# Optimization experiments

Measured on AMD Instinct MI355X. Metric: run time of the kernel, lower is better.

## Reference

```python
import jax, jax.numpy as jnp
import numpy as np

L = 7          # window side (odd)
A = 0.3        # weight of average term
B = 0.7        # weight of differential term


def mex_hat(d):
    grid = (np.mgrid[:d, :d] - d // 2) * 1.0
    eucl = np.sqrt((grid ** 2).sum(0)) / d
    return (eucl * np.exp(-eucl)).astype(np.float32)  # (d, d)


def setup_inputs() -> dict:
    key = jax.random.key(0)
    x = jax.random.normal(key, (64, 1, 512, 512), dtype=jnp.float32)
    kernel = jnp.asarray(mex_hat(L).reshape(-1))  # (L*L,), matches unfold row-major order
    return {"x": x, "kernel": kernel}


def reference(x, kernel):
    # x: [B,1,n,n], kernel: [L*L]
    n = x.shape[2]
    pad = L // 2
    xp = jnp.pad(x, ((0, 0), (0, 0), (pad, pad), (pad, pad)))  # zero pad, as F.unfold
    mean_acc = jnp.zeros_like(x)
    diff_acc = jnp.zeros_like(x)
    # fixed 49-offset loop replaces the im2col buffer; each shift is a view-slice
    for i in range(L):
        for j in range(L):
            s = jax.lax.dynamic_slice(xp, (0, 0, i, j), x.shape)
            mean_acc = mean_acc + s
            diff_acc = diff_acc + kernel[i * L + j] * jax.nn.relu(s - x)
    average_term = jnp.exp(-mean_acc / (L * L))              # [B,1,n,n]
    differential_term = diff_acc                             # [B,1,n,n]
    mask = A * average_term + B * differential_term
    mask = mask / jnp.sqrt(jnp.sum(mask ** 2))               # global L2 norm
    out = jnp.where(x > mask, x, jnp.zeros_like(x))
    return out, average_term, differential_term
```

## Files before the change

### kernel.cpp

```cpp
#include <hip/hip_runtime.h>
#include <stdint.h>

#define IMG 512
constexpr int TX = 64, TY = 32, PADW = 3;
constexpr int SMW = TX + 2 * PADW;
constexpr int SMH = TY + 2 * PADW;
constexpr int SMS = SMW + 2;
constexpr float A_W = 0.3f, B_W = 0.7f;

#define W1  0.12383970f
#define W2  0.16507309f
#define W4  0.21470754f
#define W5  0.23209061f
#define W8  0.26975268f
#define W9  0.27918814f
#define W10 0.28754623f
#define W13 0.30773566f
#define W18 0.33061044f

__device__ constexpr float KW[7][7] = {
    { W18, W13, W10, W9,  W10, W13, W18 },
    { W13, W8,  W5,  W4,  W5,  W8,  W13 },
    { W10, W5,  W2,  W1,  W2,  W5,  W10 },
    { W9,  W4,  W1,  0.f, W1,  W4,  W9  },
    { W10, W5,  W2,  W1,  W2,  W5,  W10 },
    { W13, W8,  W5,  W4,  W5,  W8,  W13 },
    { W18, W13, W10, W9,  W10, W13, W18 },
};

constexpr float ksum_calc() {
    float s = 0.f;
    for (int i = 0; i < 7; ++i)
        for (int j = 0; j < 7; ++j) s += KW[i][j];
    return s;
}
constexpr float KSUM = ksum_calc();

__global__ __launch_bounds__(256) void li_pass1(
    const float* __restrict__ x,
    float* __restrict__ outMask,
    float* __restrict__ outAvg,
    float* __restrict__ outDiff,
    float* __restrict__ partials)
{
    __shared__ float sm[SMH * SMS];
    __shared__ float red[4];
    const int tid = threadIdx.x;

    const int bx = blockIdx.x, by = blockIdx.y, b = blockIdx.z;
    const size_t imgBase = (size_t)b * IMG * IMG;
    const int x0 = bx * TX, y0 = by * TY;

    for (int idx = tid; idx < SMH * SMW; idx += 256) {
        int ly = idx / SMW, lx = idx - ly * SMW;
        int gx = x0 - PADW + lx, gy = y0 - PADW + ly;
        float v = 0.f;
        if ((unsigned)gx < IMG && (unsigned)gy < IMG)
            v = x[imgBase + (size_t)gy * IMG + gx];
        sm[ly * SMS + lx] = v;
    }
    __syncthreads();

    const int tx  = tid & 63;
    const int r   = tid >> 6;
    const int ty0 = r * 8;

    float c[8], mean[8], T[8];
    #pragma unroll
    for (int k = 0; k < 8; ++k) {
        c[k] = sm[(ty0 + k + PADW) * SMS + tx + PADW];
        mean[k] = 0.f; T[k] = 0.f;
    }

    #pragma unroll
    for (int wy = 0; wy < 14; ++wy) {
        float s[7];
        const int base = (ty0 + wy) * SMS + tx;
        #pragma unroll
        for (int dx = 0; dx < 7; ++dx) s[dx] = sm[base + dx];
        float rowsum = ((s[0] + s[1]) + (s[2] + s[3])) + ((s[4] + s[5]) + s[6]);
        #pragma unroll
        for (int k = 0; k < 8; ++k) {
            const int dy = wy - k;
            if (dy >= 0 && dy < 7) {
                mean[k] += rowsum;
                #pragma unroll
                for (int dx = 0; dx < 7; ++dx) {
                    if (KW[dy][dx] != 0.f)
                        T[k] = fmaf(KW[dy][dx], fmaxf(s[dx], c[k]), T[k]);
                }
            }
        }
    }

    float local = 0.f;
    #pragma unroll
    for (int k = 0; k < 8; ++k) {
        float avg = __expf(mean[k] * (-1.f / 49.f));
        float d   = fmaf(-KSUM, c[k], T[k]);
        float m   = fmaf(A_W, avg, B_W * d);
        local = fmaf(m, m, local);
        size_t g = imgBase + (size_t)(y0 + ty0 + k) * IMG + (x0 + tx);
        outAvg[g]  = avg;
        outDiff[g] = d;
        outMask[g] = m;
    }

    float v = local;
    #pragma unroll
    for (int off = 32; off > 0; off >>= 1) v += __shfl_down(v, off);
    if ((tid & 63) == 0) red[tid >> 6] = v;
    __syncthreads();
    if (tid == 0) {
        size_t pb = ((size_t)b * gridDim.y + by) * gridDim.x + bx;
        partials[pb] = red[0] + red[1] + red[2] + red[3];
    }
}

__global__ __launch_bounds__(1024) void li_reduce(
    const float* __restrict__ partials, int n, float* __restrict__ total)
{
    __shared__ float red[16];
    int tid = threadIdx.x;
    float v = 0.f;
    for (int i = tid; i < n; i += 1024) v += partials[i];
    #pragma unroll
    for (int off = 32; off > 0; off >>= 1) v += __shfl_down(v, off);
    if ((tid & 63) == 0) red[tid >> 6] = v;
    __syncthreads();
    if (tid == 0) {
        float s = 0.f;
        #pragma unroll
        for (int i = 0; i < 16; ++i) s += red[i];
        *total = s;
    }
}

__global__ __launch_bounds__(256) void li_pass2(
    const float4* __restrict__ x, const float4* __restrict__ mask,
    float4* __restrict__ out, const float* __restrict__ total)
{
    const float inv = 1.0f / sqrtf(*total);
    int i = blockIdx.x * 256 + threadIdx.x;
    float4 xv = x[i];
    float4 mv = mask[i];
    float4 ov;
    ov.x = (xv.x > mv.x * inv) ? xv.x : 0.f;
    ov.y = (xv.y > mv.y * inv) ? xv.y : 0.f;
    ov.z = (xv.z > mv.z * inv) ? xv.z : 0.f;
    ov.w = (xv.w > mv.w * inv) ? xv.w : 0.f;
    out[i] = ov;
}

extern "C" void kernel_launch(void* const* d_in, const int* in_sizes, int n_in,
                              void* d_out, int out_size, void* d_ws, size_t ws_size,
                              hipStream_t stream)
{
    const float* x = (const float*)d_in[0];
    const int Nelem = in_sizes[0];
    const int batch = Nelem / (IMG * IMG);

    float* out     = (float*)d_out;
    float* outMask = out;
    float* outAvg  = out + (size_t)Nelem;
    float* outDiff = out + (size_t)2 * Nelem;

    float* partials = (float*)d_ws;
    const int nblocks = (IMG / TX) * (IMG / TY) * batch;
    float* total = partials + nblocks;

    dim3 g1(IMG / TX, IMG / TY, batch);
    li_pass1<<<g1, 256, 0, stream>>>(x, outMask, outAvg, outDiff, partials);
    li_reduce<<<1, 1024, 0, stream>>>(partials, nblocks, total);

    const int nvec = Nelem / 4;
    li_pass2<<<nvec / 256, 256, 0, stream>>>(
        (const float4*)x, (const float4*)outMask, (float4*)out, total);
}
```

Measured before the change: 308.0 us.

## Fuse stencil, norm reduction and threshold into one cooperative grid-sync kernel

Replaces the three-kernel pipeline with one cooperative kernel. Each block processes eight vertical tiles, keeps its mask values in registers packed as bf16 pairs, and does a grid-wide sync after writing partial sums. Every block then re-reduces the partials and applies the threshold directly, so the full-precision mask is never written to global memory and read back, and two launches go away. The costs are fewer, longer-running blocks with a high register load, and threshold comparisons made against a bf16-rounded mask, which can flip elements that lie near the threshold. The old three-kernel path stays as a fallback if the cooperative launch fails.

```diff
diff --git a/kernel.cpp b/kernel.cpp
--- a/kernel.cpp
+++ b/kernel.cpp
@@ -1,12 +1,15 @@
 #include <hip/hip_runtime.h>
+#include <hip/hip_cooperative_groups.h>
 #include <stdint.h>
 
 #define IMG 512
-constexpr int TX = 64, TY = 32, PADW = 3;
+constexpr int PADW = 3;
+constexpr float A_W = 0.3f, B_W = 0.7f;
+
+constexpr int TX = 64, TY = 32;
 constexpr int SMW = TX + 2 * PADW;
 constexpr int SMH = TY + 2 * PADW;
 constexpr int SMS = SMW + 2;
-constexpr float A_W = 0.3f, B_W = 0.7f;
 
 #define W1  0.12383970f
 #define W2  0.16507309f
@@ -36,17 +39,151 @@
 }
 constexpr float KSUM = ksum_calc();
 
-__global__ __launch_bounds__(256) void li_pass1(
+__device__ __forceinline__ float asf(unsigned u) {
+    union { unsigned u; float f; } c; c.u = u; return c.f;
+}
+__device__ __forceinline__ unsigned f2bf_bits(float f) {
+    union { float f; unsigned u; } c; c.f = f;
+    unsigned u = c.u;
+    return (u + 0x7fffu + ((u >> 16) & 1u)) >> 16;
+}
+
+__global__ __launch_bounds__(256, 4) void li_fused(
     const float* __restrict__ x,
-    float* __restrict__ outMask,
+    float* __restrict__ outThr,
     float* __restrict__ outAvg,
     float* __restrict__ outDiff,
     float* __restrict__ partials)
 {
     __shared__ float sm[SMH * SMS];
     __shared__ float red[4];
+    __shared__ float s_inv;
+
     const int tid = threadIdx.x;
-
+    const int bx = blockIdx.x, by = blockIdx.y, b = blockIdx.z;
+    const size_t imgBase = (size_t)b * IMG * IMG;
+    const int x0 = bx * TX;
+    const int yBase = by * 256;
+
+    const int tx  = tid & 63;
+    const int r   = tid >> 6;
+    const int ty0 = r * 8;
+
+    unsigned mp[32];
+    float local = 0.f;
+
+    #pragma unroll
+    for (int s = 0; s < 8; ++s) {
+        const int y0 = yBase + s * TY;
+
+        if (s > 0) __syncthreads();
+        for (int idx = tid; idx < SMH * SMW; idx += 256) {
+            int ly = idx / SMW, lx = idx - ly * SMW;
+            int gx = x0 - PADW + lx, gy = y0 - PADW + ly;
+            float v = 0.f;
+            if ((unsigned)gx < IMG && (unsigned)gy < IMG)
+                v = x[imgBase + (size_t)gy * IMG + gx];
+            sm[ly * SMS + lx] = v;
+        }
+        __syncthreads();
+
+        float c[8], mean[8], T[8];
+        #pragma unroll
+        for (int k = 0; k < 8; ++k) {
+            c[k] = sm[(ty0 + k + PADW) * SMS + tx + PADW];
+            mean[k] = 0.f; T[k] = 0.f;
+        }
+
+        #pragma unroll
+        for (int wy = 0; wy < 14; ++wy) {
+            float sv[7];
+            const int base = (ty0 + wy) * SMS + tx;
+            #pragma unroll
+            for (int dx = 0; dx < 7; ++dx) sv[dx] = sm[base + dx];
+            float rowsum = ((sv[0] + sv[1]) + (sv[2] + sv[3])) + ((sv[4] + sv[5]) + sv[6]);
+            #pragma unroll
+            for (int k = 0; k < 8; ++k) {
+                const int dy = wy - k;
+                if (dy >= 0 && dy < 7) {
+                    mean[k] += rowsum;
+                    #pragma unroll
+                    for (int dx = 0; dx < 7; ++dx) {
+                        if (KW[dy][dx] != 0.f)
+                            T[k] = fmaf(KW[dy][dx], fmaxf(sv[dx], c[k]), T[k]);
+                    }
+                }
+            }
+        }
+
+        float m8[8];
+        #pragma unroll
+        for (int k = 0; k < 8; ++k) {
+            float avg = __expf(mean[k] * (-1.f / 49.f));
+            float d   = fmaf(-KSUM, c[k], T[k]);
+            float m   = fmaf(A_W, avg, B_W * d);
+            m8[k] = m;
+            local = fmaf(m, m, local);
+            size_t g = imgBase + (size_t)(y0 + ty0 + k) * IMG + (x0 + tx);
+            outAvg[g]  = avg;
+            outDiff[g] = d;
+        }
+        #pragma unroll
+        for (int k = 0; k < 8; k += 2)
+            mp[s * 4 + k / 2] = f2bf_bits(m8[k]) | (f2bf_bits(m8[k + 1]) << 16);
+    }
+
+    {
+        float v = local;
+        #pragma unroll
+        for (int off = 32; off > 0; off >>= 1) v += __shfl_down(v, off);
+        if ((tid & 63) == 0) red[tid >> 6] = v;
+        __syncthreads();
+        if (tid == 0) {
+            int pb = (b * (int)gridDim.y + by) * (int)gridDim.x + bx;
+            partials[pb] = red[0] + red[1] + red[2] + red[3];
+        }
+    }
+
+    __threadfence();
+    cooperative_groups::this_grid().sync();
+
+    {
+        const int nPart = (int)(gridDim.x * gridDim.y * gridDim.z);
+        float v = 0.f;
+        for (int i = tid; i < nPart; i += 256) v += partials[i];
+        #pragma unroll
+        for (int off = 32; off > 0; off >>= 1) v += __shfl_down(v, off);
+        if ((tid & 63) == 0) red[tid >> 6] = v;
+        __syncthreads();
+        if (tid == 0) s_inv = 1.0f / sqrtf(red[0] + red[1] + red[2] + red[3]);
+        __syncthreads();
+    }
+    const float inv = s_inv;
+
+    #pragma unroll
+    for (int s = 0; s < 8; ++s) {
+        #pragma unroll
+        for (int k = 0; k < 8; k += 2) {
+            unsigned pk = mp[s * 4 + k / 2];
+            float m0 = asf(pk << 16);
+            float m1 = asf(pk & 0xffff0000u);
+            size_t g = imgBase + (size_t)(yBase + s * TY + ty0 + k) * IMG + (x0 + tx);
+            float xv0 = x[g];
+            float xv1 = x[g + IMG];
+            outThr[g]       = (xv0 > m0 * inv) ? xv0 : 0.f;
+            outThr[g + IMG] = (xv1 > m1 * inv) ? xv1 : 0.f;
+        }
+    }
+}
+
+__global__ __launch_bounds__(256) void li_pass1(
+    const float* __restrict__ x,
+    float* __restrict__ outMask, float* __restrict__ outAvg,
+    float* __restrict__ outDiff, float* __restrict__ partials)
+{
+    __shared__ float sm[SMH * SMS];
+    __shared__ float red[4];
+    const int tid = threadIdx.x;
     const int bx = blockIdx.x, by = blockIdx.y, b = blockIdx.z;
     const size_t imgBase = (size_t)b * IMG * IMG;
     const int x0 = bx * TX, y0 = by * TY;
@@ -61,8 +198,8 @@
     }
     __syncthreads();
 
-    const int tx  = tid & 63;
-    const int r   = tid >> 6;
+    const int tx = tid & 63;
+    const int r  = tid >> 6;
     const int ty0 = r * 8;
 
     float c[8], mean[8], T[8];
@@ -71,28 +208,25 @@
         c[k] = sm[(ty0 + k + PADW) * SMS + tx + PADW];
         mean[k] = 0.f; T[k] = 0.f;
     }
-
     #pragma unroll
     for (int wy = 0; wy < 14; ++wy) {
-        float s[7];
+        float sv[7];
         const int base = (ty0 + wy) * SMS + tx;
         #pragma unroll
-        for (int dx = 0; dx < 7; ++dx) s[dx] = sm[base + dx];
-        float rowsum = ((s[0] + s[1]) + (s[2] + s[3])) + ((s[4] + s[5]) + s[6]);
+        for (int dx = 0; dx < 7; ++dx) sv[dx] = sm[base + dx];
+        float rowsum = ((sv[0] + sv[1]) + (sv[2] + sv[3])) + ((sv[4] + sv[5]) + sv[6]);
         #pragma unroll
         for (int k = 0; k < 8; ++k) {
             const int dy = wy - k;
             if (dy >= 0 && dy < 7) {
                 mean[k] += rowsum;
                 #pragma unroll
-                for (int dx = 0; dx < 7; ++dx) {
+                for (int dx = 0; dx < 7; ++dx)
                     if (KW[dy][dx] != 0.f)
-                        T[k] = fmaf(KW[dy][dx], fmaxf(s[dx], c[k]), T[k]);
-                }
+                        T[k] = fmaf(KW[dy][dx], fmaxf(sv[dx], c[k]), T[k]);
             }
         }
     }
-
     float local = 0.f;
     #pragma unroll
     for (int k = 0; k < 8; ++k) {
@@ -101,11 +235,8 @@
         float m   = fmaf(A_W, avg, B_W * d);
         local = fmaf(m, m, local);
         size_t g = imgBase + (size_t)(y0 + ty0 + k) * IMG + (x0 + tx);
-        outAvg[g]  = avg;
-        outDiff[g] = d;
-        outMask[g] = m;
-    }
-
+        outAvg[g] = avg; outDiff[g] = d; outMask[g] = m;
+    }
     float v = local;
     #pragma unroll
     for (int off = 32; off > 0; off >>= 1) v += __shfl_down(v, off);
@@ -161,19 +292,27 @@
     const int batch = Nelem / (IMG * IMG);
 
     float* out     = (float*)d_out;
-    float* outMask = out;
     float* outAvg  = out + (size_t)Nelem;
     float* outDiff = out + (size_t)2 * Nelem;
-
     float* partials = (float*)d_ws;
-    const int nblocks = (IMG / TX) * (IMG / TY) * batch;
-    float* total = partials + nblocks;
-
-    dim3 g1(IMG / TX, IMG / TY, batch);
-    li_pass1<<<g1, 256, 0, stream>>>(x, outMask, outAvg, outDiff, partials);
-    li_reduce<<<1, 1024, 0, stream>>>(partials, nblocks, total);
-
-    const int nvec = Nelem / 4;
-    li_pass2<<<nvec / 256, 256, 0, stream>>>(
-        (const float4*)x, (const float4*)outMask, (float4*)out, total);
-}
+
+    dim3 gridF(IMG / TX, IMG / 256, batch);
+    dim3 blockF(256, 1, 1);
+    void* args[] = { (void*)&x, (void*)&out, (void*)&outAvg,
+                     (void*)&outDiff, (void*)&partials };
+    hipError_t err = hipLaunchCooperativeKernel(
+        (const void*)li_fused, gridF, blockF, args, 0, stream);
+
+    if (err != hipSuccess) {
+        (void)hipGetLastError();
+        float* outMask = out;
+        const int nblocks = (IMG / TX) * (IMG / TY) * batch;
+        float* total = partials + nblocks;
+        dim3 g1(IMG / TX, IMG / TY, batch);
+        li_pass1<<<g1, 256, 0, stream>>>(x, outMask, outAvg, outDiff, partials);
+        li_reduce<<<1, 1024, 0, stream>>>(partials, nblocks, total);
+        const int nvec = Nelem / 4;
+        li_pass2<<<nvec / 256, 256, 0, stream>>>(
+            (const float4*)x, (const float4*)outMask, (float4*)out, total);
+    }
+}
```

Measured after the change: 610.9 us. 1.98x slower.

## Register-block 4x4 outputs per thread with float4 LDS and global access

Applied to the files above, without the earlier changes.

Each thread now computes a 4x4 output patch from a 128x32 tile instead of an 8x1 column. Shared-memory rows are loaded and read with float4 vectors, row sums are computed with a sliding window, and outputs are written as float4. This is meant to cut LDS traffic per output and global instruction count. In exchange it raises register pressure (48 accumulators) under a launch-bounds occupancy hint and adds a separate halo load path.

```diff
diff --git a/kernel.cpp b/kernel.cpp
--- a/kernel.cpp
+++ b/kernel.cpp
@@ -2,10 +2,9 @@
 #include <stdint.h>
 
 #define IMG 512
-constexpr int TX = 64, TY = 32, PADW = 3;
-constexpr int SMW = TX + 2 * PADW;
+constexpr int TX = 128, TY = 32, PADW = 3;
+constexpr int SMC = 136;
 constexpr int SMH = TY + 2 * PADW;
-constexpr int SMS = SMW + 2;
 constexpr float A_W = 0.3f, B_W = 0.7f;
 
 #define W1  0.12383970f
@@ -36,58 +35,82 @@
 }
 constexpr float KSUM = ksum_calc();
 
-__global__ __launch_bounds__(256) void li_pass1(
+__global__ __launch_bounds__(256, 4) void li_pass1(
     const float* __restrict__ x,
     float* __restrict__ outMask,
     float* __restrict__ outAvg,
     float* __restrict__ outDiff,
     float* __restrict__ partials)
 {
-    __shared__ float sm[SMH * SMS];
+    __shared__ float sm[SMH * SMC];
     __shared__ float red[4];
     const int tid = threadIdx.x;
-
     const int bx = blockIdx.x, by = blockIdx.y, b = blockIdx.z;
     const size_t imgBase = (size_t)b * IMG * IMG;
     const int x0 = bx * TX, y0 = by * TY;
 
-    for (int idx = tid; idx < SMH * SMW; idx += 256) {
-        int ly = idx / SMW, lx = idx - ly * SMW;
-        int gx = x0 - PADW + lx, gy = y0 - PADW + ly;
+    for (int idx = tid; idx < SMH * 32; idx += 256) {
+        int row = idx >> 5, c4 = idx & 31;
+        int gy = y0 - PADW + row;
+        float4 v = make_float4(0.f, 0.f, 0.f, 0.f);
+        if ((unsigned)gy < IMG)
+            v = *(const float4*)(x + imgBase + (size_t)gy * IMG + x0 + 4 * c4);
+        *(float4*)(sm + row * SMC + 4 * c4 + 4) = v;
+    }
+    if (tid < SMH * 6) {
+        int row = tid / 6, h = tid - row * 6;
+        int lx = (h < 3) ? (h - 3) : (TX + h - 3);
+        int gx = x0 + lx, gy = y0 - PADW + row;
         float v = 0.f;
         if ((unsigned)gx < IMG && (unsigned)gy < IMG)
             v = x[imgBase + (size_t)gy * IMG + gx];
-        sm[ly * SMS + lx] = v;
+        sm[row * SMC + lx + 4] = v;
     }
     __syncthreads();
 
-    const int tx  = tid & 63;
-    const int r   = tid >> 6;
-    const int ty0 = r * 8;
-
-    float c[8], mean[8], T[8];
-    #pragma unroll
-    for (int k = 0; k < 8; ++k) {
-        c[k] = sm[(ty0 + k + PADW) * SMS + tx + PADW];
-        mean[k] = 0.f; T[k] = 0.f;
-    }
-
-    #pragma unroll
-    for (int wy = 0; wy < 14; ++wy) {
-        float s[7];
-        const int base = (ty0 + wy) * SMS + tx;
-        #pragma unroll
-        for (int dx = 0; dx < 7; ++dx) s[dx] = sm[base + dx];
-        float rowsum = ((s[0] + s[1]) + (s[2] + s[3])) + ((s[4] + s[5]) + s[6]);
-        #pragma unroll
-        for (int k = 0; k < 8; ++k) {
+    const int tg  = tid & 31;
+    const int tyg = tid >> 5;
+    const int colBase = 4 * tg;
+
+    float c[4][4];
+    #pragma unroll
+    for (int k = 0; k < 4; ++k) {
+        float4 cv = *(const float4*)(sm + (tyg * 4 + k + 3) * SMC + colBase + 4);
+        c[k][0] = cv.x; c[k][1] = cv.y; c[k][2] = cv.z; c[k][3] = cv.w;
+    }
+
+    float mean[4][4], T[4][4];
+    #pragma unroll
+    for (int k = 0; k < 4; ++k)
+        #pragma unroll
+        for (int j = 0; j < 4; ++j) { mean[k][j] = 0.f; T[k][j] = 0.f; }
+
+    #pragma unroll
+    for (int wy = 0; wy < 10; ++wy) {
+        const float* rp = sm + (tyg * 4 + wy) * SMC + colBase;
+        float4 a  = *(const float4*)(rp);
+        float4 b4 = *(const float4*)(rp + 4);
+        float4 d4 = *(const float4*)(rp + 8);
+        float sv[12] = { a.x, a.y, a.z, a.w, b4.x, b4.y, b4.z, b4.w,
+                         d4.x, d4.y, d4.z, d4.w };
+        float R[4];
+        R[0] = ((sv[1] + sv[2]) + (sv[3] + sv[4])) + ((sv[5] + sv[6]) + sv[7]);
+        R[1] = R[0] - sv[1] + sv[8];
+        R[2] = R[1] - sv[2] + sv[9];
+        R[3] = R[2] - sv[3] + sv[10];
+
+        #pragma unroll
+        for (int k = 0; k < 4; ++k) {
             const int dy = wy - k;
             if (dy >= 0 && dy < 7) {
-                mean[k] += rowsum;
                 #pragma unroll
-                for (int dx = 0; dx < 7; ++dx) {
-                    if (KW[dy][dx] != 0.f)
-                        T[k] = fmaf(KW[dy][dx], fmaxf(s[dx], c[k]), T[k]);
+                for (int j = 0; j < 4; ++j) {
+                    mean[k][j] += R[j];
+                    #pragma unroll
+                    for (int dx = 0; dx < 7; ++dx) {
+                        if (KW[dy][dx] != 0.f)
+                            T[k][j] = fmaf(KW[dy][dx], fmaxf(sv[1 + j + dx], c[k][j]), T[k][j]);
+                    }
                 }
             }
         }
@@ -95,15 +118,21 @@
 
     float local = 0.f;
     #pragma unroll
-    for (int k = 0; k < 8; ++k) {
-        float avg = __expf(mean[k] * (-1.f / 49.f));
-        float d   = fmaf(-KSUM, c[k], T[k]);
-        float m   = fmaf(A_W, avg, B_W * d);
-        local = fmaf(m, m, local);
-        size_t g = imgBase + (size_t)(y0 + ty0 + k) * IMG + (x0 + tx);
-        outAvg[g]  = avg;
-        outDiff[g] = d;
-        outMask[g] = m;
+    for (int k = 0; k < 4; ++k) {
+        float4 av, dv, mv;
+        float* avp = &av.x; float* dvp = &dv.x; float* mvp = &mv.x;
+        #pragma unroll
+        for (int j = 0; j < 4; ++j) {
+            float avg = __expf(mean[k][j] * (-1.f / 49.f));
+            float d   = fmaf(-KSUM, c[k][j], T[k][j]);
+            float m   = fmaf(A_W, avg, B_W * d);
+            avp[j] = avg; dvp[j] = d; mvp[j] = m;
+            local = fmaf(m, m, local);
+        }
+        size_t g = imgBase + (size_t)(y0 + tyg * 4 + k) * IMG + (x0 + 4 * tg);
+        *(float4*)(outAvg  + g) = av;
+        *(float4*)(outDiff + g) = dv;
+        *(float4*)(outMask + g) = mv;
     }
 
     float v = local;
@@ -112,7 +141,7 @@
     if ((tid & 63) == 0) red[tid >> 6] = v;
     __syncthreads();
     if (tid == 0) {
-        size_t pb = ((size_t)b * gridDim.y + by) * gridDim.x + bx;
+        int pb = (b * (int)gridDim.y + by) * (int)gridDim.x + bx;
         partials[pb] = red[0] + red[1] + red[2] + red[3];
     }
 }
```

Result: slower. 341.2 us (+10.8%).
